# Kernel optimization log

Measured on AMD Instinct MI355X. Metric: run time of the kernel, lower is better.

## Reference

```python
import jax, jax.numpy as jnp
import numpy as np

EPS = 1e-5

def _bn(x, g, b):
    # BatchNorm1d in training mode: batch statistics over nodes
    m = jnp.mean(x, axis=0)
    v = jnp.var(x, axis=0)
    return g * (x - m) * jax.lax.rsqrt(v + EPS) + b

def _gconv(x, adj, W, b):
    # GraphConvolution: adj @ x @ W + b
    return adj @ (x @ W) + b

def _gsage(x, adj, W, b):
    # GraphSAGE layer: relu(adj @ x @ W + b)
    return jax.nn.relu(adj @ (x @ W) + b)

def setup_inputs() -> dict:
    key = jax.random.key(0)
    ks = jax.random.split(key, 20)
    N = 8192
    x = jax.random.normal(ks[0], (N, 18), dtype=jnp.float32)
    adj = jax.random.uniform(ks[1], (N, N), dtype=jnp.float32)
    s = 0.1
    p = {
        'W1': jax.random.normal(ks[2], (18, 16)) * s, 'b1': jnp.zeros((16,)),
        'W2': jax.random.normal(ks[3], (16, 16)) * s, 'b2': jnp.zeros((16,)),
        'We1': jax.random.normal(ks[4], (16, 8)) * s, 'be1': jnp.zeros((8,)),
        'Wp1': jax.random.normal(ks[5], (16, 20)) * s, 'bp1': jnp.zeros((20,)),
        'W3': jax.random.normal(ks[6], (8, 8)) * s, 'b3': jnp.zeros((8,)),
        'We2': jax.random.normal(ks[7], (8, 8)) * s, 'be2': jnp.zeros((8,)),
        'g1': jnp.ones((16,)), 'bt1': jnp.zeros((16,)),
        'g2': jnp.ones((16,)), 'bt2': jnp.zeros((16,)),
        'g3': jnp.ones((8,)), 'bt3': jnp.zeros((8,)),
    }
    p = {k: v.astype(jnp.float32) for k, v in p.items()}
    return {'x': x, 'adj': adj, **p}

def reference(x, adj, W1, b1, W2, b2, We1, be1, Wp1, bp1, W3, b3, We2, be2,
              g1, bt1, g2, bt2, g3, bt3):
    h = _bn(_gsage(x, adj, W1, b1), g1, bt1)          # [N,16]
    h = _bn(_gsage(h, adj, W2, b2), g2, bt2)          # [N,16]
    # DiffPool(16, 20, 8)
    z = _gconv(h, adj, We1, be1)                      # [N,8]
    s_l = jax.nn.softmax(_gconv(h, adj, Wp1, bp1), axis=1)  # [N,20]
    h = s_l.T @ z                                     # [20,8]
    a = s_l.T @ adj @ s_l                             # [20,20]
    h = _bn(_gsage(h, a, W3, b3), g3, bt3)            # [20,8]
    # DiffPool(8, 1, 8, is_final=True): s = ones -> column sum
    z = _gconv(h, a, We2, be2)                        # [20,8]
    return jnp.sum(z, axis=0, keepdims=True)          # [1,8]
```

## Files before the change

### kernel.cpp

```cpp
#include <hip/hip_runtime.h>
#include <cstddef>

#define NROWS 8192
constexpr float BN_EPS = 1e-5f;

typedef __attribute__((ext_vector_type(8))) short bf16x8;
typedef __attribute__((ext_vector_type(4))) float f32x4;
typedef __attribute__((ext_vector_type(2))) float f32x2;
typedef __attribute__((ext_vector_type(4))) unsigned int u32x4;

__device__ __forceinline__ unsigned short bf16u(float f) {
    unsigned u = __float_as_uint(f);
    u += 0x7FFFu + ((u >> 16) & 1u);
    return (unsigned short)(u >> 16);
}

constexpr size_t OFF_P   = 0;
constexpr size_t OFF_YP  = OFF_P   + (size_t)16 * NROWS * 32;
constexpr size_t OFF_SLP = OFF_YP  + (size_t)NROWS * 32 / 2;
constexpr size_t OFF_U   = OFF_SLP + (size_t)NROWS * 32 / 2;
constexpr size_t OFF_SL  = OFF_U   + (size_t)NROWS * 16;
constexpr size_t OFF_ST1 = OFF_SL  + (size_t)NROWS * 20;
constexpr size_t OFF_ST2 = OFF_ST1 + 32;
constexpr size_t OFF_HSM = OFF_ST2 + 32;
constexpr size_t OFF_AG  = OFF_HSM + 160;
constexpr size_t OFF_END_SMALL = OFF_AG + 400;
constexpr size_t OFF_ADJB = (OFF_END_SMALL + 15) & ~(size_t)15;
constexpr size_t NEED_FULL_BYTES = (OFF_ADJB + (size_t)NROWS * NROWS / 2) * 4;


__global__ __launch_bounds__(256)
void k_convert(const float* __restrict__ adjf, unsigned short* __restrict__ adjp)
{
    __shared__ unsigned short lds[16384];
    const int bid = blockIdx.x;
    const int rb = bid & 63, kc = (bid >> 6) & 15, q = bid >> 10;
    const int t = threadIdx.x, lane = t & 63, wv = t >> 6;
    const int row0 = rb * 128 + wv * 32;
    const int kbase = kc * 512 + q * 128;
    const int s_q = lane >> 4;
    const int khi = (lane >> 2) & 3;
    const int el2 = (lane & 3) * 2;

#pragma unroll 8
    for (int rr = 0; rr < 32; ++rr) {
        const f32x2 v = *(const f32x2*)(adjf + (size_t)(row0 + rr) * NROWS + kbase + lane * 2);
        const int m = rr >> 4, rA = rr & 15;
        int u = ((wv * 4 + s_q) * 2 + m) * 64 + rA + 16 * khi;
        u ^= ((u >> 4) & 3) ^ (((u >> 7) & 1) << 2);
        unsigned short* p = &lds[u * 8 + el2];
        p[0] = bf16u(v.x);
        p[1] = bf16u(v.y);
    }
    __syncthreads();

    const size_t blockbase = (size_t)(kc * 64 + rb) * 8192;
#pragma unroll
    for (int i = 0; i < 8; ++i) {
        const int flat = i * 256 + t;
        const int phys = flat ^ ((flat >> 4) & 3) ^ (((flat >> 7) & 1) << 2);
        const u32x4 d = *(const u32x4*)&lds[phys * 8];
        const int wvd = flat >> 9;
        const size_t gu = blockbase + (size_t)wvd * 2048 + (size_t)q * 512 + (flat & 511);
        *(u32x4*)(adjp + gu * 8) = d;
    }
}

template<int NT>
__global__ __launch_bounds__(256)
void k_spmm_p(const unsigned short* __restrict__ adjp,
              const unsigned short* __restrict__ ypu, float* __restrict__ P)
{
    constexpr int CP = NT * 16;
    const int rb   = blockIdx.x & 63;
    const int kc   = blockIdx.x >> 6;
    const int lane = threadIdx.x & 63;
    const int wv   = threadIdx.x >> 6;
    const int row0 = rb * 128 + wv * 32;
    const bf16x8* ap = (const bf16x8*)adjp;
    const bf16x8* yp = (const bf16x8*)ypu;
    const size_t wbase = ((size_t)(kc * 64 + rb) * 4 + wv) * 2048;

    f32x4 acc[2][NT];
#pragma unroll
    for (int m = 0; m < 2; ++m)
#pragma unroll
        for (int n = 0; n < NT; ++n) acc[m][n] = (f32x4){0.f, 0.f, 0.f, 0.f};

    auto LA = [&](int m, int s) -> bf16x8 {
        return ap[wbase + (size_t)s * 128 + m * 64 + lane];
    };
    auto LB = [&](int n, int s) -> bf16x8 {
        return yp[((size_t)((kc * 16 + s) * NT + n)) * 64 + lane];
    };

    bf16x8 a0 = LA(0, 0), a1 = LA(1, 0);
    bf16x8 b0 = LB(0, 0), b1;
    if constexpr (NT == 2) b1 = LB(1, 0);

#pragma unroll
    for (int s = 0; s < 16; ++s) {
        bf16x8 na0, na1, nb0, nb1;
        if (s < 15) {
            na0 = LA(0, s + 1); na1 = LA(1, s + 1);
            nb0 = LB(0, s + 1);
            if constexpr (NT == 2) nb1 = LB(1, s + 1);
        }
        acc[0][0] = __builtin_amdgcn_mfma_f32_16x16x32_bf16(a0, b0, acc[0][0], 0, 0, 0);
        acc[1][0] = __builtin_amdgcn_mfma_f32_16x16x32_bf16(a1, b0, acc[1][0], 0, 0, 0);
        if constexpr (NT == 2) {
            acc[0][1] = __builtin_amdgcn_mfma_f32_16x16x32_bf16(a0, b1, acc[0][1], 0, 0, 0);
            acc[1][1] = __builtin_amdgcn_mfma_f32_16x16x32_bf16(a1, b1, acc[1][1], 0, 0, 0);
        }
        if (s < 15) { a0 = na0; a1 = na1; b0 = nb0; if constexpr (NT == 2) b1 = nb1; }
    }

    float* Pk = P + ((size_t)kc * NROWS + row0) * CP;
    const int drow = (lane >> 4) * 4;
    const int dcol = lane & 15;
#pragma unroll
    for (int m = 0; m < 2; ++m)
#pragma unroll
        for (int n = 0; n < NT; ++n)
#pragma unroll
            for (int r = 0; r < 4; ++r)
                Pk[(size_t)(m * 16 + drow + r) * CP + n * 16 + dcol] = acc[m][n][r];
}

template<int NT>
__global__ __launch_bounds__(256)
void k_spmm_f32(const float* __restrict__ adjf,
                const unsigned short* __restrict__ ypu, float* __restrict__ P)
{
    constexpr int CP = NT * 16;
    const int rb   = blockIdx.x & 63;
    const int kc   = blockIdx.x >> 6;
    const int lane = threadIdx.x & 63;
    const int wv   = threadIdx.x >> 6;
    const int row0 = rb * 128 + wv * 32;
    const int k0   = kc * 512;
    const int rA   = lane & 15;
    const int kA   = (lane >> 4) * 8;
    const bf16x8* yp = (const bf16x8*)ypu;

    f32x4 acc[2][NT];
#pragma unroll
    for (int m = 0; m < 2; ++m)
#pragma unroll
        for (int n = 0; n < NT; ++n) acc[m][n] = (f32x4){0.f, 0.f, 0.f, 0.f};

    const size_t offA0 = (size_t)(row0 + rA) * NROWS + k0 + kA;
    const size_t offA1 = offA0 + (size_t)16 * NROWS;

    auto LA = [&](int m, int s) -> bf16x8 {
        const size_t o = (m ? offA1 : offA0) + (size_t)s * 32;
        const f32x4 u = *(const f32x4*)(adjf + o);
        const f32x4 v = *(const f32x4*)(adjf + o + 4);
        bf16x8 tt;
        tt[0] = (short)bf16u(u.x); tt[1] = (short)bf16u(u.y);
        tt[2] = (short)bf16u(u.z); tt[3] = (short)bf16u(u.w);
        tt[4] = (short)bf16u(v.x); tt[5] = (short)bf16u(v.y);
        tt[6] = (short)bf16u(v.z); tt[7] = (short)bf16u(v.w);
        return tt;
    };
    auto LB = [&](int n, int s) -> bf16x8 {
        return yp[((size_t)((kc * 16 + s) * NT + n)) * 64 + lane];
    };

    bf16x8 a0 = LA(0, 0), a1 = LA(1, 0);
    bf16x8 b0 = LB(0, 0), b1;
    if constexpr (NT == 2) b1 = LB(1, 0);

#pragma unroll
    for (int s = 0; s < 16; ++s) {
        bf16x8 na0, na1, nb0, nb1;
        if (s < 15) {
            na0 = LA(0, s + 1); na1 = LA(1, s + 1);
            nb0 = LB(0, s + 1);
            if constexpr (NT == 2) nb1 = LB(1, s + 1);
        }
        acc[0][0] = __builtin_amdgcn_mfma_f32_16x16x32_bf16(a0, b0, acc[0][0], 0, 0, 0);
        acc[1][0] = __builtin_amdgcn_mfma_f32_16x16x32_bf16(a1, b0, acc[1][0], 0, 0, 0);
        if constexpr (NT == 2) {
            acc[0][1] = __builtin_amdgcn_mfma_f32_16x16x32_bf16(a0, b1, acc[0][1], 0, 0, 0);
            acc[1][1] = __builtin_amdgcn_mfma_f32_16x16x32_bf16(a1, b1, acc[1][1], 0, 0, 0);
        }
        if (s < 15) { a0 = na0; a1 = na1; b0 = nb0; if constexpr (NT == 2) b1 = nb1; }
    }

    float* Pk = P + ((size_t)kc * NROWS + row0) * CP;
    const int drow = (lane >> 4) * 4;
    const int dcol = lane & 15;
#pragma unroll
    for (int m = 0; m < 2; ++m)
#pragma unroll
        for (int n = 0; n < NT; ++n)
#pragma unroll
            for (int r = 0; r < 4; ++r)
                Pk[(size_t)(m * 16 + drow + r) * CP + n * 16 + dcol] = acc[m][n][r];
}

__global__ __launch_bounds__(256)
void k_y1_pack(const float* __restrict__ x, const float* __restrict__ W1,
               unsigned short* __restrict__ yp)
{
    const int j = blockIdx.x * 256 + threadIdx.x;
    float xr[18];
#pragma unroll
    for (int d = 0; d < 18; ++d) xr[d] = x[j * 18 + d];
    const int kb = j >> 5, lhi = ((j & 31) >> 3) << 4, idx = j & 7;
#pragma unroll
    for (int c = 0; c < 16; ++c) {
        float a = 0.f;
#pragma unroll
        for (int d = 0; d < 18; ++d) a = fmaf(xr[d], W1[d * 16 + c], a);
        yp[((size_t)kb * 64 + (lhi | c)) * 8 + idx] = bf16u(a);
    }
}

__global__ __launch_bounds__(256)
void k_reduce16(const float* __restrict__ P, const float* __restrict__ bias,
                float* __restrict__ U, float* __restrict__ stats)
{
    const int t = threadIdx.x, col = t & 15, rg = t >> 4;
    float s = 0.f, ss = 0.f;
    for (int r = blockIdx.x * 16 + rg; r < NROWS; r += 1024) {
        float v = bias[col];
#pragma unroll
        for (int kc = 0; kc < 16; ++kc)
            v += P[((size_t)kc * NROWS + r) * 16 + col];
        v = fmaxf(v, 0.f);
        U[r * 16 + col] = v;
        s += v; ss += v * v;
    }
    __shared__ float ls[16][17], lss[16][17];
    ls[rg][col] = s; lss[rg][col] = ss;
    __syncthreads();
    if (t < 16) {
        float a = 0.f, b = 0.f;
        for (int g = 0; g < 16; ++g) { a += ls[g][t]; b += lss[g][t]; }
        atomicAdd(&stats[t], a);
        atomicAdd(&stats[16 + t], b);
    }
}

template<int COA, int COB, int NTO>
__global__ __launch_bounds__(256)
void k_bn_pack(const float* __restrict__ U, const float* __restrict__ stats,
               const float* __restrict__ g, const float* __restrict__ bt,
               const float* __restrict__ Wa, const float* __restrict__ Wb,
               unsigned short* __restrict__ yp)
{
    const int j = blockIdx.x * 256 + threadIdx.x;
    float h[16];
#pragma unroll
    for (int k = 0; k < 16; ++k) {
        const float m   = stats[k] * (1.f / NROWS);
        const float var = stats[16 + k] * (1.f / NROWS) - m * m;
        const float sc  = g[k] * rsqrtf(var + BN_EPS);
        h[k] = fmaf(U[j * 16 + k], sc, bt[k] - m * sc);
    }
    const int kb = j >> 5, lhi = ((j & 31) >> 3) << 4, idx = j & 7;
    auto slot = [&](int c) -> size_t {
        return ((size_t)(kb * NTO + (c >> 4)) * 64 + (lhi | (c & 15))) * 8 + idx;
    };
#pragma unroll
    for (int co = 0; co < COA; ++co) {
        float a = 0.f;
#pragma unroll
        for (int k = 0; k < 16; ++k) a = fmaf(h[k], Wa[k * COA + co], a);
        yp[slot(co)] = bf16u(a);
    }
#pragma unroll
    for (int co = 0; co < COB; ++co) {
        float a = 0.f;
#pragma unroll
        for (int k = 0; k < 16; ++k) a = fmaf(h[k], Wb[k * COB + co], a);
        yp[slot(COA + co)] = bf16u(a);
    }
#pragma unroll
    for (int c = COA + COB; c < NTO * 16; ++c) yp[slot(c)] = 0;
}

__global__ __launch_bounds__(256)
void k_red_fin3(const float* __restrict__ P, const float* __restrict__ be1,
                const float* __restrict__ bp1, float* __restrict__ sl,
                unsigned short* __restrict__ slp, float* __restrict__ hsm)
{
    __shared__ float szl[256 * 8];
    __shared__ float ssl[256 * 20];
    const int t = threadIdx.x;
    const int row = blockIdx.x * 256 + t;

    float s3[28];
#pragma unroll
    for (int c = 0; c < 28; ++c) s3[c] = 0.f;
#pragma unroll
    for (int kc = 0; kc < 16; ++kc) {
        const float* pr = &P[((size_t)kc * NROWS + row) * 32];
#pragma unroll
        for (int q = 0; q < 7; ++q) {
            const f32x4 v = *(const f32x4*)(pr + q * 4);
            s3[q * 4 + 0] += v.x; s3[q * 4 + 1] += v.y;
            s3[q * 4 + 2] += v.z; s3[q * 4 + 3] += v.w;
        }
    }
#pragma unroll
    for (int k = 0; k < 8; ++k) szl[t * 8 + k] = s3[k] + be1[k];

    float s[20];
    float mx = -1e30f;
#pragma unroll
    for (int k = 0; k < 20; ++k) {
        s[k] = s3[8 + k] + bp1[k];
        mx = fmaxf(mx, s[k]);
    }
    float se = 0.f;
#pragma unroll
    for (int k = 0; k < 20; ++k) { s[k] = expf(s[k] - mx); se += s[k]; }
    const float inv = 1.f / se;
    const int kb = row >> 5, lhi = ((row & 31) >> 3) << 4, idx = row & 7;
    auto slot = [&](int c) -> size_t {
        return ((size_t)(kb * 2 + (c >> 4)) * 64 + (lhi | (c & 15))) * 8 + idx;
    };
#pragma unroll
    for (int k = 0; k < 20; ++k) {
        s[k] *= inv;
        sl[(size_t)row * 20 + k] = s[k];
        ssl[t * 20 + k] = s[k];
        slp[slot(k)] = bf16u(s[k]);
    }
#pragma unroll
    for (int c = 20; c < 32; ++c) slp[slot(c)] = 0;
    __syncthreads();
    if (t < 160) {
        const int p = t >> 3, q = t & 7;
        float a = 0.f;
        for (int r = 0; r < 256; ++r) a = fmaf(ssl[r * 20 + p], szl[r * 8 + q], a);
        atomicAdd(&hsm[t], a);
    }
}

__global__ __launch_bounds__(256)
void k_red_fin4(const float* __restrict__ P, const float* __restrict__ sl,
                float* __restrict__ a_g)
{
    __shared__ float stt[256 * 20];
    __shared__ float ssl[256 * 20];
    const int t = threadIdx.x;
    const int row = blockIdx.x * 256 + t;

    float t4[20];
#pragma unroll
    for (int c = 0; c < 20; ++c) t4[c] = 0.f;
#pragma unroll
    for (int kc = 0; kc < 16; ++kc) {
        const float* pr = &P[((size_t)kc * NROWS + row) * 32];
#pragma unroll
        for (int q = 0; q < 5; ++q) {
            const f32x4 v = *(const f32x4*)(pr + q * 4);
            t4[q * 4 + 0] += v.x; t4[q * 4 + 1] += v.y;
            t4[q * 4 + 2] += v.z; t4[q * 4 + 3] += v.w;
        }
    }
#pragma unroll
    for (int c = 0; c < 20; ++c) {
        stt[t * 20 + c] = t4[c];
        ssl[t * 20 + c] = sl[(size_t)row * 20 + c];
    }
    __syncthreads();
    for (int pair = t; pair < 400; pair += 256) {
        const int p = pair / 20, q = pair % 20;
        float a = 0.f;
        for (int r = 0; r < 256; ++r) a = fmaf(ssl[r * 20 + p], stt[r * 20 + q], a);
        atomicAdd(&a_g[pair], a);
    }
}

__global__ __launch_bounds__(256)
void k_final(const float* __restrict__ hsm, const float* __restrict__ a_g,
             const float* __restrict__ W3, const float* __restrict__ b3,
             const float* __restrict__ g3, const float* __restrict__ bt3,
             const float* __restrict__ We2, const float* __restrict__ be2,
             float* __restrict__ out)
{
    __shared__ float m1[160], qb[160], hb[160], sc[8], sh[8];
    const int t = threadIdx.x;
    const int p = t >> 3, k = t & 7;
    if (t < 160) {
        float a = 0.f;
        for (int j = 0; j < 8; ++j) a = fmaf(hsm[p * 8 + j], W3[j * 8 + k], a);
        m1[t] = a;
    }
    __syncthreads();
    if (t < 160) {
        float a = b3[k];
        for (int j = 0; j < 20; ++j) a = fmaf(a_g[p * 20 + j], m1[j * 8 + k], a);
        qb[t] = fmaxf(a, 0.f);
    }
    __syncthreads();
    if (t < 8) {
        float m = 0.f, v = 0.f;
        for (int r = 0; r < 20; ++r) { float q = qb[r * 8 + t]; m += q; v += q * q; }
        m *= (1.f / 20.f); v = v * (1.f / 20.f) - m * m;
        const float s = g3[t] * rsqrtf(v + BN_EPS);
        sc[t] = s; sh[t] = bt3[t] - m * s;
    }
    __syncthreads();
    if (t < 160) hb[t] = fmaf(qb[t], sc[k], sh[k]);
    __syncthreads();
    if (t < 160) {
        float a = 0.f;
        for (int j = 0; j < 8; ++j) a = fmaf(hb[p * 8 + j], We2[j * 8 + k], a);
        m1[t] = a;
    }
    __syncthreads();
    if (t < 160) {
        float a = be2[k];
        for (int j = 0; j < 20; ++j) a = fmaf(a_g[p * 20 + j], m1[j * 8 + k], a);
        qb[t] = a;
    }
    __syncthreads();
    if (t < 8) {
        float a = 0.f;
        for (int r = 0; r < 20; ++r) a += qb[r * 8 + t];
        out[t] = a;
    }
}

extern "C" void kernel_launch(void* const* d_in, const int* in_sizes, int n_in,
                              void* d_out, int out_size, void* d_ws, size_t ws_size,
                              hipStream_t stream)
{
    const float* x   = (const float*)d_in[0];
    const float* adj = (const float*)d_in[1];
    const float* W1  = (const float*)d_in[2];
    const float* b1  = (const float*)d_in[3];
    const float* W2  = (const float*)d_in[4];
    const float* b2  = (const float*)d_in[5];
    const float* We1 = (const float*)d_in[6];
    const float* be1 = (const float*)d_in[7];
    const float* Wp1 = (const float*)d_in[8];
    const float* bp1 = (const float*)d_in[9];
    const float* W3  = (const float*)d_in[10];
    const float* b3  = (const float*)d_in[11];
    const float* We2 = (const float*)d_in[12];
    const float* be2 = (const float*)d_in[13];
    const float* g1  = (const float*)d_in[14];
    const float* bt1 = (const float*)d_in[15];
    const float* g2  = (const float*)d_in[16];
    const float* bt2 = (const float*)d_in[17];
    const float* g3  = (const float*)d_in[18];
    const float* bt3 = (const float*)d_in[19];

    float* ws = (float*)d_ws;
    float* P  = ws + OFF_P;
    unsigned short* YP   = (unsigned short*)(ws + OFF_YP);
    unsigned short* SLP  = (unsigned short*)(ws + OFF_SLP);
    float* U   = ws + OFF_U;
    float* SL  = ws + OFF_SL;
    float* ST1 = ws + OFF_ST1;
    float* ST2 = ws + OFF_ST2;
    float* HSM = ws + OFF_HSM;
    float* AG  = ws + OFF_AG;
    unsigned short* ADJP = (unsigned short*)(ws + OFF_ADJB);
    float* out = (float*)d_out;

    const bool FULL = ws_size >= NEED_FULL_BYTES;
    const dim3 blk(256);

    (void)hipMemsetAsync(ST1, 0, (32 + 32 + 160 + 400) * sizeof(float), stream);

    if (FULL) k_convert<<<4096, blk, 0, stream>>>(adj, ADJP);

    k_y1_pack<<<32, blk, 0, stream>>>(x, W1, YP);
    if (FULL) k_spmm_p<1><<<1024, blk, 0, stream>>>(ADJP, YP, P);
    else      k_spmm_f32<1><<<1024, blk, 0, stream>>>(adj, YP, P);
    k_reduce16<<<64, blk, 0, stream>>>(P, b1, U, ST1);
    k_bn_pack<16, 0, 1><<<32, blk, 0, stream>>>(U, ST1, g1, bt1, W2, nullptr, YP);

    if (FULL) k_spmm_p<1><<<1024, blk, 0, stream>>>(ADJP, YP, P);
    else      k_spmm_f32<1><<<1024, blk, 0, stream>>>(adj, YP, P);
    k_reduce16<<<64, blk, 0, stream>>>(P, b2, U, ST2);
    k_bn_pack<8, 20, 2><<<32, blk, 0, stream>>>(U, ST2, g2, bt2, We1, Wp1, YP);

    if (FULL) k_spmm_p<2><<<1024, blk, 0, stream>>>(ADJP, YP, P);
    else      k_spmm_f32<2><<<1024, blk, 0, stream>>>(adj, YP, P);
    k_red_fin3<<<32, blk, 0, stream>>>(P, be1, bp1, SL, SLP, HSM);

    if (FULL) k_spmm_p<2><<<1024, blk, 0, stream>>>(ADJP, SLP, P);
    else      k_spmm_f32<2><<<1024, blk, 0, stream>>>(adj, SLP, P);
    k_red_fin4<<<32, blk, 0, stream>>>(P, SL, AG);

    k_final<<<1, blk, 0, stream>>>(HSM, AG, W3, b3, g3, bt3, We2, be2, out);
}
```

Before: 238.4 us.

## Fuse adjacency bf16 conversion with first SpMM pass

```diff
diff --git a/kernel.cpp b/kernel.cpp
--- a/kernel.cpp
+++ b/kernel.cpp
@@ -30,39 +30,67 @@
 
 
 __global__ __launch_bounds__(256)
-void k_convert(const float* __restrict__ adjf, unsigned short* __restrict__ adjp)
+void k_conv_spmm(const float* __restrict__ adjf, unsigned short* __restrict__ adjp,
+                 const unsigned short* __restrict__ ypu, float* __restrict__ P)
 {
     __shared__ unsigned short lds[16384];
     const int bid = blockIdx.x;
-    const int rb = bid & 63, kc = (bid >> 6) & 15, q = bid >> 10;
+    const int rb = bid & 63, kc = bid >> 6;
     const int t = threadIdx.x, lane = t & 63, wv = t >> 6;
     const int row0 = rb * 128 + wv * 32;
-    const int kbase = kc * 512 + q * 128;
     const int s_q = lane >> 4;
     const int khi = (lane >> 2) & 3;
     const int el2 = (lane & 3) * 2;
-
+    const bf16x8* ap = (const bf16x8*)lds;
+    const bf16x8* yp = (const bf16x8*)ypu;
+    const size_t blockbase = (size_t)(kc * 64 + rb) * 8192;
+
+    f32x4 acc0 = (f32x4){0.f,0.f,0.f,0.f}, acc1 = (f32x4){0.f,0.f,0.f,0.f};
+
+    for (int q = 0; q < 4; ++q) {
+        const int kbase = kc * 512 + q * 128;
+        __syncthreads();
 #pragma unroll 8
-    for (int rr = 0; rr < 32; ++rr) {
-        const f32x2 v = *(const f32x2*)(adjf + (size_t)(row0 + rr) * NROWS + kbase + lane * 2);
-        const int m = rr >> 4, rA = rr & 15;
-        int u = ((wv * 4 + s_q) * 2 + m) * 64 + rA + 16 * khi;
-        u ^= ((u >> 4) & 3) ^ (((u >> 7) & 1) << 2);
-        unsigned short* p = &lds[u * 8 + el2];
-        p[0] = bf16u(v.x);
-        p[1] = bf16u(v.y);
-    }
-    __syncthreads();
-
-    const size_t blockbase = (size_t)(kc * 64 + rb) * 8192;
-#pragma unroll
-    for (int i = 0; i < 8; ++i) {
-        const int flat = i * 256 + t;
-        const int phys = flat ^ ((flat >> 4) & 3) ^ (((flat >> 7) & 1) << 2);
-        const u32x4 d = *(const u32x4*)&lds[phys * 8];
-        const int wvd = flat >> 9;
-        const size_t gu = blockbase + (size_t)wvd * 2048 + (size_t)q * 512 + (flat & 511);
-        *(u32x4*)(adjp + gu * 8) = d;
+        for (int rr = 0; rr < 32; ++rr) {
+            const f32x2 v = *(const f32x2*)(adjf + (size_t)(row0 + rr) * NROWS + kbase + lane * 2);
+            const int m = rr >> 4, rA = rr & 15;
+            int u = ((wv * 4 + s_q) * 2 + m) * 64 + rA + 16 * khi;
+            u ^= ((u >> 4) & 3) ^ (((u >> 7) & 1) << 2);
+            unsigned short* p = &lds[u * 8 + el2];
+            p[0] = bf16u(v.x);
+            p[1] = bf16u(v.y);
+        }
+        __syncthreads();
+#pragma unroll
+        for (int i = 0; i < 8; ++i) {
+            const int flat = i * 256 + t;
+            const int phys = flat ^ ((flat >> 4) & 3) ^ (((flat >> 7) & 1) << 2);
+            const u32x4 d = *(const u32x4*)&lds[phys * 8];
+            const int wvd = flat >> 9;
+            const size_t gu = blockbase + (size_t)wvd * 2048 + (size_t)q * 512 + (flat & 511);
+            *(u32x4*)(adjp + gu * 8) = d;
+        }
+#pragma unroll
+        for (int sq = 0; sq < 4; ++sq) {
+            int L0 = ((wv * 4 + sq) * 2 + 0) * 64 + lane;
+            int L1 = L0 + 64;
+            L0 ^= ((L0 >> 4) & 3) ^ (((L0 >> 7) & 1) << 2);
+            L1 ^= ((L1 >> 4) & 3) ^ (((L1 >> 7) & 1) << 2);
+            const bf16x8 a0 = ap[L0];
+            const bf16x8 a1 = ap[L1];
+            const bf16x8 b0 = yp[((size_t)(kc * 16 + q * 4 + sq)) * 64 + lane];
+            acc0 = __builtin_amdgcn_mfma_f32_16x16x32_bf16(a0, b0, acc0, 0, 0, 0);
+            acc1 = __builtin_amdgcn_mfma_f32_16x16x32_bf16(a1, b0, acc1, 0, 0, 0);
+        }
+    }
+
+    float* Pk = P + ((size_t)kc * NROWS + row0) * 16;
+    const int drow = (lane >> 4) * 4;
+    const int dcol = lane & 15;
+#pragma unroll
+    for (int r = 0; r < 4; ++r) {
+        Pk[(size_t)(drow + r) * 16 + dcol]      = acc0[r];
+        Pk[(size_t)(16 + drow + r) * 16 + dcol] = acc1[r];
     }
 }
 
@@ -471,10 +499,8 @@
 
     (void)hipMemsetAsync(ST1, 0, (32 + 32 + 160 + 400) * sizeof(float), stream);
 
-    if (FULL) k_convert<<<4096, blk, 0, stream>>>(adj, ADJP);
-
     k_y1_pack<<<32, blk, 0, stream>>>(x, W1, YP);
-    if (FULL) k_spmm_p<1><<<1024, blk, 0, stream>>>(ADJP, YP, P);
+    if (FULL) k_conv_spmm<<<1024, blk, 0, stream>>>(adj, ADJP, YP, P);
     else      k_spmm_f32<1><<<1024, blk, 0, stream>>>(adj, YP, P);
     k_reduce16<<<64, blk, 0, stream>>>(P, b1, U, ST1);
     k_bn_pack<16, 0, 1><<<32, blk, 0, stream>>>(U, ST1, g1, bt1, W2, nullptr, YP);
```

New measurement: 221.5 us. -7.1%, faster.
